# Kernel optimization log

Measured on AMD Instinct MI355X. Metric: run time of the kernel, lower is better.

## Reference

```python
import jax, jax.numpy as jnp
import numpy as np

N = 50000      # nodes
E = 800000     # edges (avg degree 16)
IN = 128       # in_feats
OUT = 128      # out_feats
H = 8          # num_heads
D = OUT // H   # out_heads (per-head dim) = 16


def _xavier(key, shape, fan_in, fan_out):
    bound = np.sqrt(6.0 / (fan_in + fan_out)).astype(np.float32)
    return jax.random.uniform(key, shape, jnp.float32, -bound, bound)


def setup_inputs() -> dict:
    key = jax.random.key(0)
    ks = jax.random.split(key, 12)
    feat = jax.random.normal(ks[0], (N, IN), jnp.float32)
    src = jax.random.randint(ks[1], (E,), 0, N, jnp.int32)
    dst = jax.random.randint(ks[2], (E,), 0, N, jnp.int32)
    # stacked per-head Linear weights: nn.Linear(IN, D) per head -> [H, IN, D]
    Wq = _xavier(ks[3], (H, IN, D), IN, D)
    Wk = _xavier(ks[4], (H, IN, D), IN, D)
    Wv = _xavier(ks[5], (H, IN, D), IN, D)
    b = 1.0 / np.sqrt(IN).astype(np.float32)
    bq = jax.random.uniform(ks[6], (H, D), jnp.float32, -b, b)
    bk = jax.random.uniform(ks[7], (H, D), jnp.float32, -b, b)
    bv = jax.random.uniform(ks[8], (H, D), jnp.float32, -b, b)
    # residual self projection W_self: Linear(IN, OUT), stored as [IN, OUT]
    Ws = _xavier(ks[9], (IN, OUT), IN, OUT)
    bs = jax.random.uniform(ks[10], (OUT,), jnp.float32, -b, b)
    return {"feat": feat, "src": src, "dst": dst,
            "Wq": Wq, "bq": bq, "Wk": Wk, "bk": bk, "Wv": Wv, "bv": bv,
            "Ws": Ws, "bs": bs}


def reference(feat, src, dst, Wq, bq, Wk, bk, Wv, bv, Ws, bs):
    # per-head projections, all heads at once: [N, H, D]
    q = jnp.einsum('ni,hid->nhd', feat, Wq) + bq
    k = jnp.einsum('ni,hid->nhd', feat, Wk) + bk
    v = jnp.einsum('ni,hid->nhd', feat, Wv) + bv

    # edge scores: sum_d k[src] * q[dst], scaled by sqrt(D)  -> [E, H]
    scores = jnp.einsum('ehd,ehd->eh', k[src], q[dst]) / np.sqrt(D).astype(np.float32)

    # edge_softmax: segment softmax over incoming edges of each dst node
    m = jax.ops.segment_max(scores, dst, num_segments=N)          # [N, H]
    m = jax.lax.stop_gradient(jnp.where(jnp.isfinite(m), m, 0.0))
    ex = jnp.exp(scores - m[dst])                                  # [E, H]
    den = jax.ops.segment_sum(ex, dst, num_segments=N)            # [N, H]
    attn = ex / den[dst]                                           # [E, H]

    # weighted scatter-sum aggregation: h[dst] += attn * v[src]
    msg = v[src] * attn[:, :, None]                                # [E, H, D]
    h = jax.ops.segment_sum(msg, dst, num_segments=N)              # [N, H, D]

    rst = h.reshape(N, H * D)
    # residual: W_self(feat_dst)
    rst = rst + feat @ Ws + bs
    return rst
```

## Files before the change

### kernel.cpp

```cpp
#include <hip/hip_runtime.h>
#include <hip/hip_bf16.h>

typedef unsigned short u16;
typedef unsigned int u32;
typedef __attribute__((ext_vector_type(4))) unsigned int uint4v;
typedef __bf16 bf16x8 __attribute__((ext_vector_type(8)));
typedef float f32x4 __attribute__((ext_vector_type(4)));

#define INF 128
#define OUTF 128
#define NHEAD 8
#define HDIM 16
#define CAP 48
#define NBUCK 196
#define BSHIFT 8
#define BNODES 256
#define BCAP 4608
#define ECHUNK 4096

__device__ __forceinline__ float lo2f(u32 u) { return __uint_as_float(u << 16); }
__device__ __forceinline__ float hi2f(u32 u) { return __uint_as_float(u & 0xffff0000u); }
__device__ __forceinline__ float bf2f(u16 b) { return __uint_as_float(((u32)b) << 16); }
__device__ __forceinline__ u16 f2bf(float x) {
    __hip_bfloat16 h = __float2bfloat16(x);
    return *reinterpret_cast<u16*>(&h);
}
__device__ __forceinline__ float fast_exp2(float x) {
    return __builtin_amdgcn_exp2f(x);
}

__device__ __forceinline__ void load8(const void* base, size_t eoff, int isf32, float o[8]) {
    if (isf32) {
        const float* p = (const float*)base + eoff;
        float4 a = *(const float4*)p;
        float4 b = *(const float4*)(p + 4);
        o[0] = a.x; o[1] = a.y; o[2] = a.z; o[3] = a.w;
        o[4] = b.x; o[5] = b.y; o[6] = b.z; o[7] = b.w;
    } else {
        uint4v u = *(const uint4v*)((const u16*)base + eoff);
        o[0] = lo2f(u.x); o[1] = hi2f(u.x);
        o[2] = lo2f(u.y); o[3] = hi2f(u.y);
        o[4] = lo2f(u.z); o[5] = hi2f(u.z);
        o[6] = lo2f(u.w); o[7] = hi2f(u.w);
    }
}

__device__ __forceinline__ uint4v pack8(const float v[8]) {
    uint4v u;
    u.x = (u32)f2bf(v[0]) | ((u32)f2bf(v[1]) << 16);
    u.y = (u32)f2bf(v[2]) | ((u32)f2bf(v[3]) << 16);
    u.z = (u32)f2bf(v[4]) | ((u32)f2bf(v[5]) << 16);
    u.w = (u32)f2bf(v[6]) | ((u32)f2bf(v[7]) << 16);
    return u;
}

__device__ __forceinline__ f32x4 mfma16(bf16x8 a, bf16x8 b, f32x4 c) {
    return __builtin_amdgcn_mfma_f32_16x16x32_bf16(a, b, c, 0, 0, 0);
}

__global__ __launch_bounds__(256) void prep_kernel(
    const u32* __restrict__ featw,
    const void* __restrict__ Wq, const void* __restrict__ bq,
    const void* __restrict__ Wk, const void* __restrict__ bk,
    const void* __restrict__ Wv, const void* __restrict__ bv,
    const void* __restrict__ Ws, const void* __restrict__ bs,
    u16* __restrict__ Wcat, float* __restrict__ bcat, int* __restrict__ flag,
    int* __restrict__ bucketCursor)
{
    __shared__ int sflag;
    const int tid = threadIdx.x;
    if (tid < 64) {
        float mx = 0.f;
#pragma unroll
        for (int i = 0; i < 4; ++i) {
            u32 u = featw[tid * 4 + i];
            float a = fabsf(lo2f(u));
            float b = fabsf(hi2f(u));
            if (!(a < 1e30f)) a = 1e30f;
            if (!(b < 1e30f)) b = 1e30f;
            mx = fmaxf(mx, fmaxf(a, b));
        }
#pragma unroll
        for (int off = 32; off; off >>= 1) mx = fmaxf(mx, __shfl_xor(mx, off));
        if (tid == 0) sflag = (mx > 1e6f) ? 1 : 0;
    }
    __syncthreads();
    const int isf32 = sflag;
    if (blockIdx.x == 0 && tid == 0) *flag = isf32;

    const int wi = blockIdx.x * 256 + tid;
    if (wi < NBUCK) bucketCursor[wi] = 0;

    const int col = wi >> 4, ch = wi & 15;
    const int mat = col >> 7, c = col & 127;
    const void* W = (mat == 0) ? Wq : (mat == 1) ? Wk : (mat == 2) ? Wv : Ws;
    const void* bb = (mat == 0) ? bq : (mat == 1) ? bk : (mat == 2) ? bv : bs;
    size_t base; int stride;
    if (mat < 3) { int h = c >> 4, d = c & 15; base = (size_t)h * (INF * HDIM) + d; stride = HDIM; }
    else { base = c; stride = OUTF; }
#pragma unroll
    for (int j = 0; j < 8; ++j) {
        int i = ch * 8 + j;
        float w = isf32 ? ((const float*)W)[base + (size_t)i * stride]
                        : bf2f(((const u16*)W)[base + (size_t)i * stride]);
        Wcat[(size_t)col * INF + i] = f2bf(w);
    }
    if (ch == 0) bcat[col] = isf32 ? ((const float*)bb)[c] : bf2f(((const u16*)bb)[c]);
}

__global__ __launch_bounds__(256) void proj_kernel(
    const void* __restrict__ feat, const u16* __restrict__ Wcat,
    const float* __restrict__ bcat,
    u16* __restrict__ qb, u16* __restrict__ kb, u16* __restrict__ vb,
    void* __restrict__ outp, const int* __restrict__ flag, int N)
{
    __shared__ uint4v smem4[64 * 16];
    const int tid = threadIdx.x;
    const int isf32 = *flag;
    char* sb = (char*)smem4;
    const int n0 = blockIdx.x * 64;

    {
        int row = tid >> 2;
        int k0 = (tid & 3) * 32;
        int rowg = n0 + row; if (rowg >= N) rowg = N - 1;
        size_t goff = (size_t)rowg * INF + k0;
#pragma unroll
        for (int m = 0; m < 4; ++m) {
            float t[8];
            load8(feat, goff + m * 8, isf32, t);
            uint4v pk = pack8(t);
            int kbyte = 2 * (k0 + m * 8);
            int off = row * 256 + (kbyte ^ ((row & 7) << 4));
            *(uint4v*)(sb + off) = pk;
        }
    }
    __syncthreads();

    const int l = tid & 63, w = tid >> 6;
    const int lrow = l & 15, lk = l >> 4;
    const int j = lrow;

    bf16x8 af[4][4];
#pragma unroll
    for (int rt = 0; rt < 4; ++rt) {
        int row = rt * 16 + lrow;
#pragma unroll
        for (int ks = 0; ks < 4; ++ks) {
            int kbyte = ks * 64 + lk * 16;
            int off = row * 256 + (kbyte ^ ((row & 7) << 4));
            af[rt][ks] = *(const bf16x8*)(sb + off);
        }
    }

    const u16* wb = Wcat + (size_t)(w * 128 + lrow) * INF + lk * 8;
    float biases[8];
#pragma unroll
    for (int ct = 0; ct < 8; ++ct) biases[ct] = bcat[w * 128 + ct * 16 + lrow];

    u32* bp = (w == 0) ? (u32*)qb : (w == 1) ? (u32*)kb
             : (w == 2) ? (u32*)vb : (u32*)outp;
    const int src16 = (j & 7) * 2;

    bf16x8 buf0[8], buf1[8];
#pragma unroll
    for (int ks = 0; ks < 4; ++ks) {
        buf0[ks]     = *(const bf16x8*)(wb + (size_t)0 * 16 * INF + ks * 32);
        buf0[4 + ks] = *(const bf16x8*)(wb + (size_t)1 * 16 * INF + ks * 32);
    }

#pragma unroll
    for (int ctp = 0; ctp < 4; ++ctp) {
        const int ctA = 2 * ctp, ctB = 2 * ctp + 1;
        bf16x8* cur = (ctp & 1) ? buf1 : buf0;
        bf16x8* nxt = (ctp & 1) ? buf0 : buf1;
        if (ctp < 3) {
            const int nA = 2 * (ctp + 1), nB = nA + 1;
#pragma unroll
            for (int ks = 0; ks < 4; ++ks) {
                nxt[ks]     = *(const bf16x8*)(wb + (size_t)nA * 16 * INF + ks * 32);
                nxt[4 + ks] = *(const bf16x8*)(wb + (size_t)nB * 16 * INF + ks * 32);
            }
        }
        f32x4 accA[4] = {{0,0,0,0},{0,0,0,0},{0,0,0,0},{0,0,0,0}};
        f32x4 accB[4] = {{0,0,0,0},{0,0,0,0},{0,0,0,0},{0,0,0,0}};
#pragma unroll
        for (int ks = 0; ks < 4; ++ks)
#pragma unroll
            for (int rt = 0; rt < 4; ++rt) {
                accA[rt] = mfma16(af[rt][ks], cur[ks], accA[rt]);
                accB[rt] = mfma16(af[rt][ks], cur[4 + ks], accB[rt]);
            }

        float biasA = biases[ctA], biasB = biases[ctB];
#pragma unroll
        for (int rt = 0; rt < 4; ++rt) {
#pragma unroll
            for (int r = 0; r < 4; ++r) {
                int node = n0 + rt * 16 + lk * 4 + r;
                float vA = accA[rt][r] + biasA;
                float vB = accB[rt][r] + biasB;
                if (w == 3 && isf32) {
                    if (node < N) {
                        ((float*)outp)[(size_t)node * OUTF + ctA * 16 + lrow] = vA;
                        ((float*)outp)[(size_t)node * OUTF + ctB * 16 + lrow] = vB;
                    }
                } else {
                    float pvA = __shfl_xor(vA, 1);
                    float pvB = __shfl_xor(vB, 1);
                    u32 pkA = (u32)f2bf(vA) | ((u32)f2bf(pvA) << 16);
                    u32 pkB = (u32)f2bf(vB) | ((u32)f2bf(pvB) << 16);
                    u32 a = __shfl(pkA, src16, 16);
                    u32 b = __shfl(pkB, src16, 16);
                    u32 val = (j & 8) ? b : a;
                    if (node < N) bp[(size_t)node * 64 + ctp * 16 + j] = val;
                }
            }
        }
    }
}

__global__ __launch_bounds__(256) void part_kernel(
    const int* __restrict__ dst, const int* __restrict__ srcv,
    int* __restrict__ bucketCursor, u32* __restrict__ bucketArr, int E)
{
    __shared__ int hist[NBUCK], gbase[NBUCK], hist2[NBUCK];
    const int tid = threadIdx.x;
    const int e0 = blockIdx.x * ECHUNK;

    for (int i = tid; i < NBUCK; i += 256) { hist[i] = 0; hist2[i] = 0; }
    __syncthreads();
#pragma unroll
    for (int i = 0; i < 16; ++i) {
        int e = e0 + i * 256 + tid;
        if (e < E) atomicAdd(&hist[dst[e] >> BSHIFT], 1);
    }
    __syncthreads();
    for (int i = tid; i < NBUCK; i += 256)
        gbase[i] = atomicAdd(&bucketCursor[i], hist[i]);
    __syncthreads();
#pragma unroll
    for (int i = 0; i < 16; ++i) {
        int e = e0 + i * 256 + tid;
        if (e < E) {
            int d = dst[e], s = srcv[e];
            int b = d >> BSHIFT;
            int loc = atomicAdd(&hist2[b], 1);
            int idx = gbase[b] + loc;
            if (idx < BCAP)
                bucketArr[(size_t)b * BCAP + idx] =
                    ((u32)(d & (BNODES - 1)) << 16) | (u32)s;
        }
    }
}

__global__ __launch_bounds__(256) void csr_kernel(
    const u32* __restrict__ bucketArr, const int* __restrict__ bucketCursor,
    int* __restrict__ cursor, u16* __restrict__ srcs16, int N)
{
    __shared__ int cnt[BNODES];
    __shared__ u16 seg[BNODES * CAP];
    const int b = blockIdx.x;
    const int tid = threadIdx.x;
    const int nodeBase = b << BSHIFT;

    for (int i = tid; i < BNODES; i += 256) cnt[i] = 0;
    __syncthreads();

    int m = bucketCursor[b]; if (m > BCAP) m = BCAP;
    const u32* ap = bucketArr + (size_t)b * BCAP;
    for (int i = tid; i < m; i += 256) {
        u32 pr = ap[i];
        int dloc = pr >> 16;
        int pos = atomicAdd(&cnt[dloc], 1);
        if (pos < CAP) seg[dloc * CAP + pos] = (u16)(pr & 0xffffu);
    }
    __syncthreads();

    uint4v* so = (uint4v*)(srcs16 + (size_t)nodeBase * CAP);
    const uint4v* si = (const uint4v*)seg;
    const int nvec = BNODES * CAP / 8;
    for (int i = tid; i < nvec; i += 256) so[i] = si[i];
    for (int i = tid; i < BNODES; i += 256) {
        int n = nodeBase + i;
        if (n < N) cursor[n] = cnt[i];
    }
}

__global__ __launch_bounds__(256) void attn_kernel(
    const u16* __restrict__ qb, const u16* __restrict__ kb, const u16* __restrict__ vb,
    const int* __restrict__ cursor, const u16* __restrict__ srcs16,
    void* __restrict__ outp, const int* __restrict__ flag, int N)
{
    const int n = blockIdx.x * 4 + (threadIdx.x >> 6);
    if (n >= N) return;
    const int isf32 = *flag;
    const int lane = threadIdx.x & 63;

    const u32* __restrict__ kdw = (const u32*)kb;
    const u32* __restrict__ vdw = (const u32*)vb;

    const float C = 0.36067376022224085f;
    const u32 qu = ((const u32*)qb)[(size_t)n * 64 + lane];
    const float q0 = lo2f(qu) * C, q1 = hi2f(qu) * C;

    int cnt = cursor[n]; if (cnt > CAP) cnt = CAP;
    const u16* sp = srcs16 + (size_t)n * CAP;

    float den = 0.f, a0 = 0.f, a1 = 0.f;
    int p = 0;
    for (; p + 8 <= cnt; p += 8) {
        int s[8];
#pragma unroll
        for (int j = 0; j < 8; ++j) s[j] = sp[p + j];
        u32 ku[8], vu[8];
#pragma unroll
        for (int j = 0; j < 8; ++j) {
            ku[j] = kdw[(size_t)s[j] * 64 + lane];
            vu[j] = vdw[(size_t)s[j] * 64 + lane];
        }
        float pr[8];
#pragma unroll
        for (int j = 0; j < 8; ++j) pr[j] = fmaf(hi2f(ku[j]), q1, lo2f(ku[j]) * q0);
#pragma unroll
        for (int off = 1; off < 8; off <<= 1)
#pragma unroll
            for (int j = 0; j < 8; ++j) pr[j] += __shfl_xor(pr[j], off);
#pragma unroll
        for (int j = 0; j < 8; ++j) {
            float e = fast_exp2(pr[j]);
            den += e;
            a0 = fmaf(e, lo2f(vu[j]), a0);
            a1 = fmaf(e, hi2f(vu[j]), a1);
        }
    }
    for (; p < cnt; ++p) {
        int s = sp[p];
        u32 ku = kdw[(size_t)s * 64 + lane];
        u32 vu = vdw[(size_t)s * 64 + lane];
        float pr = fmaf(hi2f(ku), q1, lo2f(ku) * q0);
        pr += __shfl_xor(pr, 1); pr += __shfl_xor(pr, 2); pr += __shfl_xor(pr, 4);
        float e = fast_exp2(pr);
        den += e;
        a0 = fmaf(e, lo2f(vu), a0);
        a1 = fmaf(e, hi2f(vu), a1);
    }
    float inv = (den > 0.f) ? (1.0f / den) : 0.f;
    float r0 = a0 * inv, r1 = a1 * inv;
    if (isf32) {
        float2* op = (float2*)outp + (size_t)n * 64 + lane;
        float2 o = *op; o.x += r0; o.y += r1; *op = o;
    } else {
        u32* op = (u32*)outp + (size_t)n * 64 + lane;
        u32 ou = *op;
        u32 pk = (u32)f2bf(lo2f(ou) + r0) | ((u32)f2bf(hi2f(ou) + r1) << 16);
        *op = pk;
    }
}

extern "C" void kernel_launch(void* const* d_in, const int* in_sizes, int n_in,
                              void* d_out, int out_size, void* d_ws, size_t ws_size,
                              hipStream_t stream) {
    const void* feat = d_in[0];
    const int* src  = (const int*)d_in[1];
    const int* dst  = (const int*)d_in[2];
    const void* Wq = d_in[3]; const void* bq = d_in[4];
    const void* Wk = d_in[5]; const void* bk = d_in[6];
    const void* Wv = d_in[7]; const void* bv = d_in[8];
    const void* Ws = d_in[9]; const void* bs = d_in[10];

    const int N = in_sizes[0] / INF;
    const int E = in_sizes[1];

    u16* qb = (u16*)d_ws;
    u16* kb = qb + (size_t)N * OUTF;
    u16* vb = kb + (size_t)N * OUTF;
    u16* Wcat = vb + (size_t)N * OUTF;
    float* bcat = (float*)(Wcat + 512 * INF);
    int* cursor  = (int*)(bcat + 512);
    int* flag    = cursor + N;
    int* bucketCursor = flag + 1;
    u16* srcs16  = (u16*)(bucketCursor + NBUCK);
    u32* bucketArr = (u32*)(srcs16 + (size_t)NBUCK * BNODES * CAP);

    const int projBlocks = (N + 63) / 64;
    const int partBlocks = (E + ECHUNK - 1) / ECHUNK;

    prep_kernel<<<32, 256, 0, stream>>>((const u32*)feat, Wq, bq, Wk, bk, Wv, bv, Ws, bs,
                                        Wcat, bcat, flag, bucketCursor);
    proj_kernel<<<projBlocks, 256, 0, stream>>>(feat, Wcat, bcat, qb, kb, vb,
                                                d_out, flag, N);
    part_kernel<<<partBlocks, 256, 0, stream>>>(dst, src, bucketCursor, bucketArr, E);
    csr_kernel<<<NBUCK, 256, 0, stream>>>(bucketArr, bucketCursor, cursor, srcs16, N);
    attn_kernel<<<(N + 3) / 4, 256, 0, stream>>>(qb, kb, vb, cursor, srcs16,
                                                 d_out, flag, N);
}
```

Baseline: 137.6 us.

## Fuse independent prep/partition and projection/CSR kernels into shared launches

Merges weight preparation with edge bucket partitioning into one launch, and the QKV/self projection GEMM with the CSR bucket build into another, dispatching by block index so independent work overlaps on the GPU. Projection tiles are split into two blocks per 64-node tile, each computing half the output columns, to expose more parallelism. The bucket cursor reset moves to a hipMemsetAsync because it must precede partitioning within the fused launch. The fused projection blocks now reserve the larger CSR LDS footprint, which may reduce occupancy, and each half-tile block reloads the feature tile.

```diff
diff --git a/kernel.cpp b/kernel.cpp
--- a/kernel.cpp
+++ b/kernel.cpp
@@ -17,6 +17,7 @@
 #define BNODES 256
 #define BCAP 4608
 #define ECHUNK 4096
+#define PREPB 32
 
 __device__ __forceinline__ float lo2f(u32 u) { return __uint_as_float(u << 16); }
 __device__ __forceinline__ float hi2f(u32 u) { return __uint_as_float(u & 0xffff0000u); }
@@ -58,17 +59,51 @@
     return __builtin_amdgcn_mfma_f32_16x16x32_bf16(a, b, c, 0, 0, 0);
 }
 
-__global__ __launch_bounds__(256) void prep_kernel(
+__global__ __launch_bounds__(256) void prep_part_kernel(
     const u32* __restrict__ featw,
     const void* __restrict__ Wq, const void* __restrict__ bq,
     const void* __restrict__ Wk, const void* __restrict__ bk,
     const void* __restrict__ Wv, const void* __restrict__ bv,
     const void* __restrict__ Ws, const void* __restrict__ bs,
     u16* __restrict__ Wcat, float* __restrict__ bcat, int* __restrict__ flag,
-    int* __restrict__ bucketCursor)
+    const int* __restrict__ dst, const int* __restrict__ srcv,
+    int* __restrict__ bucketCursor, u32* __restrict__ bucketArr, int E)
 {
-    __shared__ int sflag;
+    __shared__ int lds_i[3 * NBUCK];
     const int tid = threadIdx.x;
+
+    if (blockIdx.x >= PREPB) {
+        int* hist  = lds_i;
+        int* gbase = lds_i + NBUCK;
+        int* hist2 = lds_i + 2 * NBUCK;
+        const int e0 = (blockIdx.x - PREPB) * ECHUNK;
+        for (int i = tid; i < NBUCK; i += 256) { hist[i] = 0; hist2[i] = 0; }
+        __syncthreads();
+#pragma unroll
+        for (int i = 0; i < 16; ++i) {
+            int e = e0 + i * 256 + tid;
+            if (e < E) atomicAdd(&hist[dst[e] >> BSHIFT], 1);
+        }
+        __syncthreads();
+        for (int i = tid; i < NBUCK; i += 256)
+            gbase[i] = atomicAdd(&bucketCursor[i], hist[i]);
+        __syncthreads();
+#pragma unroll
+        for (int i = 0; i < 16; ++i) {
+            int e = e0 + i * 256 + tid;
+            if (e < E) {
+                int d = dst[e], s = srcv[e];
+                int b = d >> BSHIFT;
+                int loc = atomicAdd(&hist2[b], 1);
+                int idx = gbase[b] + loc;
+                if (idx < BCAP)
+                    bucketArr[(size_t)b * BCAP + idx] =
+                        ((u32)(d & (BNODES - 1)) << 16) | (u32)s;
+            }
+        }
+        return;
+    }
+
     if (tid < 64) {
         float mx = 0.f;
 #pragma unroll
@@ -82,15 +117,13 @@
         }
 #pragma unroll
         for (int off = 32; off; off >>= 1) mx = fmaxf(mx, __shfl_xor(mx, off));
-        if (tid == 0) sflag = (mx > 1e6f) ? 1 : 0;
+        if (tid == 0) lds_i[0] = (mx > 1e6f) ? 1 : 0;
     }
     __syncthreads();
-    const int isf32 = sflag;
+    const int isf32 = lds_i[0];
     if (blockIdx.x == 0 && tid == 0) *flag = isf32;
 
     const int wi = blockIdx.x * 256 + tid;
-    if (wi < NBUCK) bucketCursor[wi] = 0;
-
     const int col = wi >> 4, ch = wi & 15;
     const int mat = col >> 7, c = col & 127;
     const void* W = (mat == 0) ? Wq : (mat == 1) ? Wk : (mat == 2) ? Wv : Ws;
@@ -108,17 +141,52 @@
     if (ch == 0) bcat[col] = isf32 ? ((const float*)bb)[c] : bf2f(((const u16*)bb)[c]);
 }
 
-__global__ __launch_bounds__(256) void proj_kernel(
+__global__ __launch_bounds__(256) void proj_csr_kernel(
     const void* __restrict__ feat, const u16* __restrict__ Wcat,
     const float* __restrict__ bcat,
     u16* __restrict__ qb, u16* __restrict__ kb, u16* __restrict__ vb,
-    void* __restrict__ outp, const int* __restrict__ flag, int N)
+    void* __restrict__ outp, const int* __restrict__ flag, int N,
+    const u32* __restrict__ bucketArr, const int* __restrict__ bucketCursor,
+    int* __restrict__ cursor, u16* __restrict__ srcs16)
 {
-    __shared__ uint4v smem4[64 * 16];
+    __shared__ __attribute__((aligned(16))) char ldsb[BNODES * 4 + BNODES * CAP * 2];
     const int tid = threadIdx.x;
+
+    if (blockIdx.x < NBUCK) {
+        int* cnt = (int*)ldsb;
+        u16* seg = (u16*)(ldsb + BNODES * 4);
+        const int b = blockIdx.x;
+        const int nodeBase = b << BSHIFT;
+
+        for (int i = tid; i < BNODES; i += 256) cnt[i] = 0;
+        __syncthreads();
+
+        int m = bucketCursor[b]; if (m > BCAP) m = BCAP;
+        const u32* ap = bucketArr + (size_t)b * BCAP;
+        for (int i = tid; i < m; i += 256) {
+            u32 pr = ap[i];
+            int dloc = pr >> 16;
+            int pos = atomicAdd(&cnt[dloc], 1);
+            if (pos < CAP) seg[dloc * CAP + pos] = (u16)(pr & 0xffffu);
+        }
+        __syncthreads();
+
+        uint4v* so = (uint4v*)(srcs16 + (size_t)nodeBase * CAP);
+        const uint4v* si = (const uint4v*)seg;
+        const int nvec = BNODES * CAP / 8;
+        for (int i = tid; i < nvec; i += 256) so[i] = si[i];
+        for (int i = tid; i < BNODES; i += 256) {
+            int n = nodeBase + i;
+            if (n < N) cursor[n] = cnt[i];
+        }
+        return;
+    }
+
+    const int pbid = blockIdx.x - NBUCK;
+    const int tile = pbid >> 1, bi = pbid & 1;
     const int isf32 = *flag;
-    char* sb = (char*)smem4;
-    const int n0 = blockIdx.x * 64;
+    char* sb = ldsb;
+    const int n0 = tile * 64;
 
     {
         int row = tid >> 2;
@@ -154,9 +222,10 @@
     }
 
     const u16* wb = Wcat + (size_t)(w * 128 + lrow) * INF + lk * 8;
-    float biases[8];
-#pragma unroll
-    for (int ct = 0; ct < 8; ++ct) biases[ct] = bcat[w * 128 + ct * 16 + lrow];
+    float biases[4];
+#pragma unroll
+    for (int ctl = 0; ctl < 4; ++ctl)
+        biases[ctl] = bcat[w * 128 + (bi * 4 + ctl) * 16 + lrow];
 
     u32* bp = (w == 0) ? (u32*)qb : (w == 1) ? (u32*)kb
              : (w == 2) ? (u32*)vb : (u32*)outp;
@@ -165,21 +234,22 @@
     bf16x8 buf0[8], buf1[8];
 #pragma unroll
     for (int ks = 0; ks < 4; ++ks) {
-        buf0[ks]     = *(const bf16x8*)(wb + (size_t)0 * 16 * INF + ks * 32);
-        buf0[4 + ks] = *(const bf16x8*)(wb + (size_t)1 * 16 * INF + ks * 32);
-    }
-
-#pragma unroll
-    for (int ctp = 0; ctp < 4; ++ctp) {
-        const int ctA = 2 * ctp, ctB = 2 * ctp + 1;
-        bf16x8* cur = (ctp & 1) ? buf1 : buf0;
-        bf16x8* nxt = (ctp & 1) ? buf0 : buf1;
-        if (ctp < 3) {
-            const int nA = 2 * (ctp + 1), nB = nA + 1;
+        buf0[ks]     = *(const bf16x8*)(wb + (size_t)(bi * 4 + 0) * 16 * INF + ks * 32);
+        buf0[4 + ks] = *(const bf16x8*)(wb + (size_t)(bi * 4 + 1) * 16 * INF + ks * 32);
+    }
+
+#pragma unroll
+    for (int ctpl = 0; ctpl < 2; ++ctpl) {
+        const int ctp = bi * 2 + ctpl;
+        const int ctA = bi * 4 + 2 * ctpl;
+        const int ctB = ctA + 1;
+        bf16x8* cur = ctpl ? buf1 : buf0;
+        bf16x8* nxt = ctpl ? buf0 : buf1;
+        if (ctpl < 1) {
 #pragma unroll
             for (int ks = 0; ks < 4; ++ks) {
-                nxt[ks]     = *(const bf16x8*)(wb + (size_t)nA * 16 * INF + ks * 32);
-                nxt[4 + ks] = *(const bf16x8*)(wb + (size_t)nB * 16 * INF + ks * 32);
+                nxt[ks]     = *(const bf16x8*)(wb + (size_t)(bi * 4 + 2) * 16 * INF + ks * 32);
+                nxt[4 + ks] = *(const bf16x8*)(wb + (size_t)(bi * 4 + 3) * 16 * INF + ks * 32);
             }
         }
         f32x4 accA[4] = {{0,0,0,0},{0,0,0,0},{0,0,0,0},{0,0,0,0}};
@@ -192,7 +262,7 @@
                 accB[rt] = mfma16(af[rt][ks], cur[4 + ks], accB[rt]);
             }
 
-        float biasA = biases[ctA], biasB = biases[ctB];
+        float biasA = biases[2 * ctpl], biasB = biases[2 * ctpl + 1];
 #pragma unroll
         for (int rt = 0; rt < 4; ++rt) {
 #pragma unroll
@@ -220,73 +290,6 @@
     }
 }
 
-__global__ __launch_bounds__(256) void part_kernel(
-    const int* __restrict__ dst, const int* __restrict__ srcv,
-    int* __restrict__ bucketCursor, u32* __restrict__ bucketArr, int E)
-{
-    __shared__ int hist[NBUCK], gbase[NBUCK], hist2[NBUCK];
-    const int tid = threadIdx.x;
-    const int e0 = blockIdx.x * ECHUNK;
-
-    for (int i = tid; i < NBUCK; i += 256) { hist[i] = 0; hist2[i] = 0; }
-    __syncthreads();
-#pragma unroll
-    for (int i = 0; i < 16; ++i) {
-        int e = e0 + i * 256 + tid;
-        if (e < E) atomicAdd(&hist[dst[e] >> BSHIFT], 1);
-    }
-    __syncthreads();
-    for (int i = tid; i < NBUCK; i += 256)
-        gbase[i] = atomicAdd(&bucketCursor[i], hist[i]);
-    __syncthreads();
-#pragma unroll
-    for (int i = 0; i < 16; ++i) {
-        int e = e0 + i * 256 + tid;
-        if (e < E) {
-            int d = dst[e], s = srcv[e];
-            int b = d >> BSHIFT;
-            int loc = atomicAdd(&hist2[b], 1);
-            int idx = gbase[b] + loc;
-            if (idx < BCAP)
-                bucketArr[(size_t)b * BCAP + idx] =
-                    ((u32)(d & (BNODES - 1)) << 16) | (u32)s;
-        }
-    }
-}
-
-__global__ __launch_bounds__(256) void csr_kernel(
-    const u32* __restrict__ bucketArr, const int* __restrict__ bucketCursor,
-    int* __restrict__ cursor, u16* __restrict__ srcs16, int N)
-{
-    __shared__ int cnt[BNODES];
-    __shared__ u16 seg[BNODES * CAP];
-    const int b = blockIdx.x;
-    const int tid = threadIdx.x;
-    const int nodeBase = b << BSHIFT;
-
-    for (int i = tid; i < BNODES; i += 256) cnt[i] = 0;
-    __syncthreads();
-
-    int m = bucketCursor[b]; if (m > BCAP) m = BCAP;
-    const u32* ap = bucketArr + (size_t)b * BCAP;
-    for (int i = tid; i < m; i += 256) {
-        u32 pr = ap[i];
-        int dloc = pr >> 16;
-        int pos = atomicAdd(&cnt[dloc], 1);
-        if (pos < CAP) seg[dloc * CAP + pos] = (u16)(pr & 0xffffu);
-    }
-    __syncthreads();
-
-    uint4v* so = (uint4v*)(srcs16 + (size_t)nodeBase * CAP);
-    const uint4v* si = (const uint4v*)seg;
-    const int nvec = BNODES * CAP / 8;
-    for (int i = tid; i < nvec; i += 256) so[i] = si[i];
-    for (int i = tid; i < BNODES; i += 256) {
-        int n = nodeBase + i;
-        if (n < N) cursor[n] = cnt[i];
-    }
-}
-
 __global__ __launch_bounds__(256) void attn_kernel(
     const u16* __restrict__ qb, const u16* __restrict__ kb, const u16* __restrict__ vb,
     const int* __restrict__ cursor, const u16* __restrict__ srcs16,
@@ -383,15 +386,17 @@
     u16* srcs16  = (u16*)(bucketCursor + NBUCK);
     u32* bucketArr = (u32*)(srcs16 + (size_t)NBUCK * BNODES * CAP);
 
-    const int projBlocks = (N + 63) / 64;
+    const int tiles = (N + 63) / 64;
+    const int projBlocks = 2 * tiles;
     const int partBlocks = (E + ECHUNK - 1) / ECHUNK;
 
-    prep_kernel<<<32, 256, 0, stream>>>((const u32*)feat, Wq, bq, Wk, bk, Wv, bv, Ws, bs,
-                                        Wcat, bcat, flag, bucketCursor);
-    proj_kernel<<<projBlocks, 256, 0, stream>>>(feat, Wcat, bcat, qb, kb, vb,
-                                                d_out, flag, N);
-    part_kernel<<<partBlocks, 256, 0, stream>>>(dst, src, bucketCursor, bucketArr, E);
-    csr_kernel<<<NBUCK, 256, 0, stream>>>(bucketArr, bucketCursor, cursor, srcs16, N);
+    (void)hipMemsetAsync(bucketCursor, 0, NBUCK * sizeof(int), stream);
+    prep_part_kernel<<<PREPB + partBlocks, 256, 0, stream>>>(
+        (const u32*)feat, Wq, bq, Wk, bk, Wv, bv, Ws, bs,
+        Wcat, bcat, flag, dst, src, bucketCursor, bucketArr, E);
+    proj_csr_kernel<<<NBUCK + projBlocks, 256, 0, stream>>>(
+        feat, Wcat, bcat, qb, kb, vb, d_out, flag, N,
+        bucketArr, bucketCursor, cursor, srcs16);
     attn_kernel<<<(N + 3) / 4, 256, 0, stream>>>(qb, kb, vb, cursor, srcs16,
                                                  d_out, flag, N);
 }
```

New measurement: 137.9 us. Within noise of the previous version (+0.2%).
